# Kernel optimization log

Hardware: AMD Instinct MI355X
Metric: run time of the kernel (lower is better)

The kernel has to match this reference:

```python
import jax, jax.numpy as jnp
import numpy as np

N = 50000
E = 800000
IN_DIM = 128
HIDDEN = 128
OUT_DIM = 64
NUM_GRAPHS = 64


def setup_inputs() -> dict:
    key = jax.random.key(0)
    ks = jax.random.split(key, 16)
    x = jax.random.normal(ks[0], (N, IN_DIM), dtype=jnp.float32)
    edge_index = jax.random.randint(ks[1], (2, E), 0, N, dtype=jnp.int32)
    batch = jnp.sort(jax.random.randint(ks[2], (N,), 0, NUM_GRAPHS, dtype=jnp.int32))

    def glorot(k, shape):
        fan_in = shape[1]
        return jax.random.normal(k, shape, dtype=jnp.float32) / jnp.sqrt(jnp.float32(fan_in))

    # SAGEConv params: lin_l (on aggregated neighbors, with bias), lin_r (on self, no bias)
    return {
        "x": x,
        "edge_index": edge_index,
        "batch": batch,
        "W1l": glorot(ks[3], (HIDDEN, IN_DIM)), "b1l": jnp.zeros((HIDDEN,), jnp.float32),
        "W1r": glorot(ks[4], (HIDDEN, IN_DIM)),
        "W2l": glorot(ks[5], (HIDDEN, HIDDEN)), "b2l": jnp.zeros((HIDDEN,), jnp.float32),
        "W2r": glorot(ks[6], (HIDDEN, HIDDEN)),
        "W3l": glorot(ks[7], (HIDDEN, HIDDEN)), "b3l": jnp.zeros((HIDDEN,), jnp.float32),
        "W3r": glorot(ks[8], (HIDDEN, HIDDEN)),
        "Wlin": glorot(ks[9], (OUT_DIM, HIDDEN)), "blin": jnp.zeros((OUT_DIM,), jnp.float32),
    }


def sage_conv(x, src, dst, Wl, bl, Wr):
    # aggr='add': scatter-add source features onto target nodes, then two linears.
    agg = jax.ops.segment_sum(x[src], dst, num_segments=N)  # [N, d_in]
    return agg @ Wl.T + bl + x @ Wr.T


def reference(x, edge_index, batch, W1l, b1l, W1r, W2l, b2l, W2r, W3l, b3l, W3r, Wlin, blin):
    src, dst = edge_index[0], edge_index[1]
    h = jax.nn.relu(sage_conv(x, src, dst, W1l, b1l, W1r))
    # dropout p=0.3 is identity at inference
    h = jax.nn.relu(sage_conv(h, src, dst, W2l, b2l, W2r))
    h = sage_conv(h, src, dst, W3l, b3l, W3r)
    # global mean pool over graphs
    sums = jax.ops.segment_sum(h, batch, num_segments=NUM_GRAPHS)  # [G, hidden]
    counts = jax.ops.segment_sum(jnp.ones((N,), h.dtype), batch, num_segments=NUM_GRAPHS)
    pooled = sums / jnp.maximum(counts, 1.0)[:, None]
    return pooled @ Wlin.T + blin  # [G, out_dim]
```

## Files before the change

kernel.cpp:

```cpp
#include <hip/hip_runtime.h>


typedef __bf16 bf16x8 __attribute__((ext_vector_type(8)));
typedef float f32x4 __attribute__((ext_vector_type(4)));
typedef float f32x2 __attribute__((ext_vector_type(2)));

#define BINB 160
#define NBMAX 512
#define CH 8192

static __device__ __forceinline__ unsigned short f2bf(float f) {
    unsigned u = __builtin_bit_cast(unsigned, f);
    return (unsigned short)((u + 0x7fffu + ((u >> 16) & 1u)) >> 16);
}
static __device__ __forceinline__ uint2 pk8_fp8(const float* f) {
    int lo = 0, hi = 0;
    lo = __builtin_amdgcn_cvt_pk_fp8_f32(f[0], f[1], lo, false);
    lo = __builtin_amdgcn_cvt_pk_fp8_f32(f[2], f[3], lo, true);
    hi = __builtin_amdgcn_cvt_pk_fp8_f32(f[4], f[5], hi, false);
    hi = __builtin_amdgcn_cvt_pk_fp8_f32(f[6], f[7], hi, true);
    return make_uint2((unsigned)lo, (unsigned)hi);
}
static __device__ __forceinline__ unsigned char f2fp8(float v) {
    return (unsigned char)(__builtin_amdgcn_cvt_pk_fp8_f32(v, v, 0, false) & 0xff);
}

__global__ __launch_bounds__(256) void k_bincast(
    const int* __restrict__ ei, int* __restrict__ cnt_mat, int E, int nb, int epb,
    const float* __restrict__ x, unsigned short* __restrict__ xb,
    unsigned char* __restrict__ x8, int n8, int nxblk,
    const float* __restrict__ W1l, const float* __restrict__ W1r,
    const float* __restrict__ W2l, const float* __restrict__ W2r,
    unsigned short* __restrict__ Whi)
{
    __shared__ int lc[NBMAX];
    int bid = blockIdx.x;
    if (bid < BINB) {
        for (int i = threadIdx.x; i < nb; i += 256) lc[i] = 0;
        __syncthreads();
        int b0 = bid * epb;
        int b1 = min(b0 + epb, E);
        for (int i = b0 + threadIdx.x; i < b1; i += 256)
            atomicAdd(&lc[ei[E + i] >> 7], 1);
        __syncthreads();
        for (int i = threadIdx.x; i < nb; i += 256)
            cnt_mat[i * BINB + bid] = lc[i];
    } else if (bid < BINB + nxblk) {
        int i = (bid - BINB) * 256 + threadIdx.x;
        if (i >= n8) return;
        float f[8];
        *(float4*)(f + 0) = *(const float4*)(x + (size_t)i * 8);
        *(float4*)(f + 4) = *(const float4*)(x + (size_t)i * 8 + 4);
        ushort4 oa, ob;
        oa.x = f2bf(f[0]); oa.y = f2bf(f[1]); oa.z = f2bf(f[2]); oa.w = f2bf(f[3]);
        ob.x = f2bf(f[4]); ob.y = f2bf(f[5]); ob.z = f2bf(f[6]); ob.w = f2bf(f[7]);
        int node = i >> 4, c = i & 15;
        size_t dstb = (size_t)(node >> 4) * 2048 + (size_t)(c >> 2) * 512
                    + (size_t)((c & 3) * 16 + (node & 15)) * 8;
        *(ushort4*)(xb + dstb) = oa;
        *(ushort4*)(xb + dstb + 4) = ob;
        *(uint2*)(x8 + (size_t)i * 8) = pk8_fp8(f);
    } else {
        int wb = bid - BINB - nxblk;
        int layer = wb >> 7;
        int j = wb & 127;
        int k = threadIdx.x;
        const float* Wl = (layer == 0) ? W1l : W2l;
        const float* Wr = (layer == 0) ? W1r : W2r;
        float w = (k < 128) ? Wl[j * 128 + k] : Wr[j * 128 + k - 128];
        int js = j >> 4, mr = j & 15;
        int s = k >> 5, quad = (k >> 3) & 3, e = k & 7;
        size_t o = (size_t)layer * 32768
                 + ((size_t)(js * 8 + s) * 64 + quad * 16 + mr) * 8 + e;
        Whi[o] = f2bf(w);
    }
}

__global__ __launch_bounds__(256) void k_mrowscan(
    const int* __restrict__ cnt_mat, int* __restrict__ rowloc, int* __restrict__ btot)
{
    __shared__ int s[256];
    int b = blockIdx.x;
    int t = threadIdx.x;
    int v = (t < BINB) ? cnt_mat[b * BINB + t] : 0;
    s[t] = v;
    __syncthreads();
#pragma unroll
    for (int off = 1; off < 256; off <<= 1) {
        int u = (t >= off) ? s[t - off] : 0;
        __syncthreads();
        s[t] += u;
        __syncthreads();
    }
    if (t < BINB) rowloc[b * BINB + t] = s[t] - v;
    if (t == 255) btot[b] = s[255];
}

__global__ __launch_bounds__(256) void k_scan2b(
    const int* __restrict__ btot, int* __restrict__ bbase, int nb, int* __restrict__ total_out)
{
    __shared__ int s[256];
    int t = threadIdx.x;
    int per = (nb + 255) / 256;
    int s0 = t * per, e0 = min(s0 + per, nb);
    int sum = 0;
    for (int i = s0; i < e0; ++i) sum += btot[i];
    s[t] = sum;
    __syncthreads();
#pragma unroll
    for (int off = 1; off < 256; off <<= 1) {
        int u = (t >= off) ? s[t - off] : 0;
        __syncthreads();
        s[t] += u;
        __syncthreads();
    }
    int run = s[t] - sum;
    for (int i = s0; i < e0; ++i) { bbase[i] = run; run += btot[i]; }
    if (t == 255) *total_out = s[255];
}

__global__ __launch_bounds__(256) void k_binscatter(
    const int* __restrict__ ei, const int* __restrict__ rowloc, const int* __restrict__ bbase,
    unsigned* __restrict__ binned, int E, int nb, int epb)
{
    __shared__ int lofs[NBMAX];
    __shared__ int lcnt[NBMAX];
    for (int i = threadIdx.x; i < nb; i += 256) {
        lofs[i] = rowloc[i * BINB + blockIdx.x] + bbase[i];
        lcnt[i] = 0;
    }
    __syncthreads();
    int b0 = blockIdx.x * epb;
    int b1 = min(b0 + epb, E);
    for (int i = b0 + threadIdx.x; i < b1; i += 256) {
        int s = ei[i];
        int d = ei[E + i];
        int b = d >> 7;
        int r = atomicAdd(&lcnt[b], 1);
        binned[lofs[b] + r] = (unsigned)s | ((unsigned)(d & 127) << 16);
    }
}

__global__ __launch_bounds__(256) void k_fillfine2(
    const unsigned* __restrict__ binned, const int* __restrict__ bbase,
    const int* __restrict__ batch, int* __restrict__ starts,
    unsigned short* __restrict__ csr_src, int* __restrict__ gestart,
    int E, int nb, int n)
{
    __shared__ int lc[128];
    __shared__ int lpos[128];
    int b = blockIdx.x;
    int t = threadIdx.x;
    int node0 = b << 7;
    int bs = bbase[b];
    int be = (b == nb - 1) ? E : bbase[b + 1];
    if (t < 128) lc[t] = 0;
    __syncthreads();
    for (int i = bs + t; i < be; i += 256)
        atomicAdd(&lc[(binned[i] >> 16) & 127], 1);
    __syncthreads();
    int v = (t < 128) ? lc[t] : 0;
    if (t < 128) lpos[t] = v;
    __syncthreads();
#pragma unroll
    for (int off = 1; off < 128; off <<= 1) {
        int u = (t >= off && t < 128) ? lpos[t - off] : 0;
        __syncthreads();
        if (t < 128) lpos[t] += u;
        __syncthreads();
    }
    int excl = (t < 128) ? (lpos[t] - v) : 0;
    __syncthreads();
    if (t < 128) {
        int node = node0 + t;
        if (node < n) {
            int st = bs + excl;
            starts[node] = st;
            int bc = batch[node];
            int bp = (node == 0) ? -1 : batch[node - 1];
            for (int g = bp + 1; g <= bc; ++g) gestart[g] = st;
            if (node == n - 1)
                for (int g = bc + 1; g <= 64; ++g) gestart[g] = E;
        }
        lpos[t] = bs + excl;
    }
    if (b == nb - 1 && t == 0) starts[n] = E;
    __syncthreads();
    for (int i = bs + t; i < be; i += 256) {
        unsigned e = binned[i];
        int slot = atomicAdd(&lpos[(e >> 16) & 127], 1);
        csr_src[slot] = (unsigned short)(e & 0xffffu);
    }
}

__global__ __launch_bounds__(256) void k_hist(
    const unsigned short* __restrict__ csr, const int* __restrict__ gestart,
    const int* __restrict__ batch, unsigned short* __restrict__ cntb,
    int n, int nsp, int nch)
{
    __shared__ unsigned lc[CH];
    int bid = blockIdx.x;
    int c = bid % nch;
    int gr = bid / nch;
    int s0 = c * CH;
    int t = threadIdx.x;
    if (gr < 64) {
        for (int i = t; i < CH; i += 256) lc[i] = 0;
        __syncthreads();
        int e0 = gestart[gr], e1 = gestart[gr + 1];
        for (int i = e0 + t; i < e1; i += 256) {
            unsigned d = (unsigned)((int)csr[i] - s0);
            if (d < (unsigned)CH) atomicAdd(&lc[d], 1u);
        }
        __syncthreads();
        for (int i = t; i < CH; i += 256) {
            int s = s0 + i;
            if (s < nsp)
                cntb[(size_t)gr * nsp + s] = f2bf((float)lc[i]);
        }
    } else {
        int g2 = gr - 64;
        for (int i = t; i < CH; i += 256) {
            int s = s0 + i;
            if (s < nsp)
                cntb[(size_t)gr * nsp + s] =
                    (s < n && batch[s] == g2) ? (unsigned short)0x3f80 : (unsigned short)0;
        }
    }
}

#define ACC8P(v)                                                        \
    do {                                                                \
        f32x2 p0 = __builtin_amdgcn_cvt_pk_f32_fp8((v).x, false);       \
        f32x2 p1 = __builtin_amdgcn_cvt_pk_f32_fp8((v).x, true);        \
        f32x2 p2 = __builtin_amdgcn_cvt_pk_f32_fp8((v).y, false);       \
        f32x2 p3 = __builtin_amdgcn_cvt_pk_f32_fp8((v).y, true);        \
        A01 += p0; A23 += p1; A45 += p2; A67 += p3;                     \
    } while (0)

#define PROC_CHUNK(idxv, cntv)                                          \
    {                                                                   \
        int j = 0;                                                      \
        for (; j + 16 <= (cntv); j += 16) {                             \
            int s0 = __shfl((int)(idxv), j + eg);                       \
            int s1 = __shfl((int)(idxv), j + 4 + eg);                   \
            int s2 = __shfl((int)(idxv), j + 8 + eg);                   \
            int s3 = __shfl((int)(idxv), j + 12 + eg);                  \
            uint2 v0 = *(const uint2*)(hrow + (size_t)s0 * 128);        \
            uint2 v1 = *(const uint2*)(hrow + (size_t)s1 * 128);        \
            uint2 v2 = *(const uint2*)(hrow + (size_t)s2 * 128);        \
            uint2 v3 = *(const uint2*)(hrow + (size_t)s3 * 128);        \
            ACC8P(v0);                                                  \
            ACC8P(v1);                                                  \
            ACC8P(v2);                                                  \
            ACC8P(v3);                                                  \
        }                                                               \
        for (; j + 4 <= (cntv); j += 4) {                               \
            int s0 = __shfl((int)(idxv), j + eg);                       \
            uint2 v0 = *(const uint2*)(hrow + (size_t)s0 * 128);        \
            ACC8P(v0);                                                  \
        }                                                               \
        if (j < (cntv)) {                                               \
            int k = j + eg;                                             \
            int sm = __shfl((int)(idxv), (k < (cntv)) ? k : ((cntv) - 1)); \
            uint2 v = *(const uint2*)(hrow + (size_t)sm * 128);         \
            if (k >= (cntv)) v = make_uint2(0u, 0u);                    \
            ACC8P(v);                                                   \
        }                                                               \
    }

#define REDUCE8()                                                       \
    a0 += __shfl_xor(a0, 16); a0 += __shfl_xor(a0, 32);                 \
    a1 += __shfl_xor(a1, 16); a1 += __shfl_xor(a1, 32);                 \
    a2 += __shfl_xor(a2, 16); a2 += __shfl_xor(a2, 32);                 \
    a3 += __shfl_xor(a3, 16); a3 += __shfl_xor(a3, 32);                 \
    a4 += __shfl_xor(a4, 16); a4 += __shfl_xor(a4, 32);                 \
    a5 += __shfl_xor(a5, 16); a5 += __shfl_xor(a5, 32);                 \
    a6 += __shfl_xor(a6, 16); a6 += __shfl_xor(a6, 32);                 \
    a7 += __shfl_xor(a7, 16); a7 += __shfl_xor(a7, 32);

__global__ __launch_bounds__(256) void k_layer(
    const unsigned char* __restrict__ h8_in, const int* __restrict__ starts,
    const unsigned short* __restrict__ csr, const unsigned short* __restrict__ hf,
    const unsigned short* __restrict__ Whi, const float* __restrict__ bl,
    unsigned short* __restrict__ outf, unsigned char* __restrict__ out8,
    unsigned short* __restrict__ h2tb,
    int n, int nsp, int mode)
{
    __shared__ unsigned short sagg[2048];
    __shared__ unsigned char s8[2048];
    int t = threadIdx.x;
    int wv = t >> 6;
    int lane = t & 63;
    int node0 = blockIdx.x * 16;

    {
        int eg = lane >> 4;
        int fb = lane & 15;
        const unsigned char* hrow = h8_in + fb * 8;
        int nodeA = node0 + wv * 4;
        int st[5];
#pragma unroll
        for (int r = 0; r < 5; ++r) {
            int nn = nodeA + r;
            st[r] = starts[nn > n ? n : nn];
        }
        unsigned idx4[4];
#pragma unroll
        for (int r = 0; r < 4; ++r)
            idx4[r] = (st[r] + lane < st[r + 1]) ? (unsigned)csr[st[r] + lane] : 0u;

#pragma unroll
        for (int r = 0; r < 4; ++r) {
            f32x2 A01 = (f32x2){0.f, 0.f}, A23 = (f32x2){0.f, 0.f},
                  A45 = (f32x2){0.f, 0.f}, A67 = (f32x2){0.f, 0.f};
            int deg = st[r + 1] - st[r];
            int c0 = min(64, deg);
            PROC_CHUNK(idx4[r], c0)
            for (int base = st[r] + 64; base < st[r + 1]; base += 64) {
                int cnt2 = min(64, st[r + 1] - base);
                unsigned idx = (base + lane < st[r + 1]) ? (unsigned)csr[base + lane] : 0u;
                PROC_CHUNK(idx, cnt2)
            }
            float a0 = A01.x, a1 = A01.y, a2 = A23.x, a3 = A23.y,
                  a4 = A45.x, a5 = A45.y, a6 = A67.x, a7 = A67.y;
            REDUCE8()
            if (eg == 0) {
                int ln = wv * 4 + r;
                unsigned u0 = (unsigned)f2bf(a0) | ((unsigned)f2bf(a1) << 16);
                unsigned u1 = (unsigned)f2bf(a2) | ((unsigned)f2bf(a3) << 16);
                unsigned u2 = (unsigned)f2bf(a4) | ((unsigned)f2bf(a5) << 16);
                unsigned u3 = (unsigned)f2bf(a6) | ((unsigned)f2bf(a7) << 16);
                size_t dst = (size_t)(fb >> 2) * 512 + (size_t)((fb & 3) * 16 + ln) * 8;
                *(uint4*)(sagg + dst) = make_uint4(u0, u1, u2, u3);
            }
        }
    }
    __syncthreads();

    int quad = lane >> 4;
    int mr = lane & 15;
    int js0 = wv * 2;

    f32x4 acc0 = (f32x4){0.f, 0.f, 0.f, 0.f};
    f32x4 acc1 = (f32x4){0.f, 0.f, 0.f, 0.f};

    const unsigned short* wp = Whi + (size_t)js0 * 4096 + (size_t)lane * 8;
    const unsigned short* sa = sagg + (size_t)lane * 8;
    const unsigned short* ha = hf + (size_t)blockIdx.x * 2048 + (size_t)lane * 8;

    uint4 pb[2][3];
#define LAYER_LOAD(s, b)                                                  \
    do {                                                                  \
        pb[b][0] = *(const uint4*)(wp + (size_t)(s) * 512);               \
        pb[b][1] = *(const uint4*)(wp + 4096 + (size_t)(s) * 512);        \
        pb[b][2] = ((s) < 4)                                              \
            ? *(const uint4*)(sa + (size_t)(s) * 512)                     \
            : *(const uint4*)(ha + (size_t)((s) - 4) * 512);              \
    } while (0)

    LAYER_LOAD(0, 0);
    LAYER_LOAD(1, 1);
#pragma unroll
    for (int s = 0; s < 8; ++s) {
        int b = s & 1;
        bf16x8 bh0 = __builtin_bit_cast(bf16x8, pb[b][0]);
        bf16x8 bh1 = __builtin_bit_cast(bf16x8, pb[b][1]);
        bf16x8 A0 = __builtin_bit_cast(bf16x8, pb[b][2]);
        acc0 = __builtin_amdgcn_mfma_f32_16x16x32_bf16(A0, bh0, acc0, 0, 0, 0);
        acc1 = __builtin_amdgcn_mfma_f32_16x16x32_bf16(A0, bh1, acc1, 0, 0, 0);
        if (s + 2 < 8) LAYER_LOAD(s + 2, b);
    }
#undef LAYER_LOAD

    float vv[2][4];
#pragma unroll
    for (int mi = 0; mi < 2; ++mi) {
        f32x4 a = mi ? acc1 : acc0;
        int col = (js0 + mi) * 16 + mr;
        float bias = bl[col];
#pragma unroll
        for (int r = 0; r < 4; ++r) {
            int node = node0 + quad * 4 + r;
            float v = fmaxf(a[r] + bias, 0.f);
            vv[mi][r] = (node < n) ? v : 0.f;
        }
    }
    __syncthreads();
    if (mode == 0) {
#pragma unroll
        for (int mi = 0; mi < 2; ++mi) {
            int col = (js0 + mi) * 16 + mr;
            int so = col >> 5, q2 = (col >> 3) & 3, e2 = col & 7;
#pragma unroll
            for (int r = 0; r < 4; ++r) {
                int nl = quad * 4 + r;
                sagg[so * 512 + (q2 * 16 + nl) * 8 + e2] = f2bf(vv[mi][r]);
                s8[nl * 128 + col] = f2fp8(vv[mi][r]);
            }
        }
        __syncthreads();
        *(uint4*)(outf + (size_t)blockIdx.x * 2048 + (size_t)t * 8) =
            *(const uint4*)(sagg + (size_t)t * 8);
        int nl = t >> 4;
        if (node0 + nl < n)
            *(uint2*)(out8 + (size_t)(node0 + nl) * 128 + (t & 15) * 8) =
                *(const uint2*)(s8 + nl * 128 + (t & 15) * 8);
    } else {
#pragma unroll
        for (int mi = 0; mi < 2; ++mi) {
            int col = (js0 + mi) * 16 + mr;
#pragma unroll
            for (int r = 0; r < 4; ++r)
                sagg[col * 16 + quad * 4 + r] = f2bf(vv[mi][r]);
        }
        __syncthreads();
        int col = t >> 1;
        *(uint4*)(h2tb + (size_t)col * nsp + node0 + (t & 1) * 8) =
            *(const uint4*)(sagg + col * 16 + (t & 1) * 8);
    }
}

__global__ __launch_bounds__(256) void k_gsum(
    const unsigned short* __restrict__ cntb, const unsigned short* __restrict__ h2tb,
    float* __restrict__ part, int nsp, int ksteps, int gb)
{
    int t = threadIdx.x;
    int wv = t >> 6, lane = t & 63;
    int fast = lane & 15;
    int kc = (lane >> 4) * 8;
    int kpb = (ksteps + gb - 1) / gb;
    int k0 = blockIdx.x * kpb, k1 = min(k0 + kpb, ksteps);

    f32x4 accE[8], accP[8];
#pragma unroll
    for (int i = 0; i < 8; ++i) {
        accE[i] = (f32x4){0.f, 0.f, 0.f, 0.f};
        accP[i] = (f32x4){0.f, 0.f, 0.f, 0.f};
    }

    const unsigned short* apE = cntb + (size_t)(wv * 16 + fast) * nsp + kc;
    const unsigned short* apP = apE + (size_t)64 * nsp;
    const unsigned short* bp  = h2tb + (size_t)fast * nsp + kc;

    if (k0 < k1) {
        int kb = k0 * 32;
        uint4 ca0 = *(const uint4*)(apE + kb);
        uint4 ca1 = *(const uint4*)(apP + kb);
        uint4 cb[8];
#pragma unroll
        for (int ft = 0; ft < 8; ++ft)
            cb[ft] = *(const uint4*)(bp + (size_t)ft * 16 * nsp + kb);
        for (int ks = k0; ks < k1; ++ks) {
            int kn = min(ks + 1, k1 - 1) * 32;
            uint4 na0 = *(const uint4*)(apE + kn);
            uint4 na1 = *(const uint4*)(apP + kn);
            uint4 nb[8];
#pragma unroll
            for (int ft = 0; ft < 8; ++ft)
                nb[ft] = *(const uint4*)(bp + (size_t)ft * 16 * nsp + kn);
            bf16x8 aE = __builtin_bit_cast(bf16x8, ca0);
            bf16x8 aP = __builtin_bit_cast(bf16x8, ca1);
#pragma unroll
            for (int ft = 0; ft < 8; ++ft) {
                bf16x8 bf = __builtin_bit_cast(bf16x8, cb[ft]);
                accE[ft] = __builtin_amdgcn_mfma_f32_16x16x32_bf16(aE, bf, accE[ft], 0, 0, 0);
                accP[ft] = __builtin_amdgcn_mfma_f32_16x16x32_bf16(aP, bf, accP[ft], 0, 0, 0);
            }
            ca0 = na0; ca1 = na1;
#pragma unroll
            for (int ft = 0; ft < 8; ++ft) cb[ft] = nb[ft];
        }
    }
    float* po = part + (size_t)blockIdx.x * 16384;
    int quad = lane >> 4, mr = lane & 15;
#pragma unroll
    for (int ft = 0; ft < 8; ++ft) {
        int col = ft * 16 + mr;
#pragma unroll
        for (int r = 0; r < 4; ++r) {
            po[(size_t)(wv * 16 + quad * 4 + r) * 128 + col] = accE[ft][r];
            po[(size_t)(64 + wv * 16 + quad * 4 + r) * 128 + col] = accP[ft][r];
        }
    }
}

__global__ __launch_bounds__(256) void k_reduce(
    const float* __restrict__ part, float* __restrict__ red, int gb)
{
    int i = blockIdx.x * 256 + threadIdx.x;
    float s0 = 0.f, s1 = 0.f, s2 = 0.f, s3 = 0.f;
    int p = 0;
    for (; p + 4 <= gb; p += 4) {
        s0 += part[(size_t)p * 16384 + i];
        s1 += part[(size_t)(p + 1) * 16384 + i];
        s2 += part[(size_t)(p + 2) * 16384 + i];
        s3 += part[(size_t)(p + 3) * 16384 + i];
    }
    for (; p < gb; ++p) s0 += part[(size_t)p * 16384 + i];
    red[i] = (s0 + s1) + (s2 + s3);
}

__global__ __launch_bounds__(128) void k_final(
    const float* __restrict__ red, const int* __restrict__ batch,
    const float* __restrict__ W3l, const float* __restrict__ b3,
    const float* __restrict__ W3r,
    const float* __restrict__ Wlin, const float* __restrict__ blin,
    float* __restrict__ out, int n)
{
    __shared__ float sE[128], sP[128], tmp[128];
    int g = blockIdx.x;
    int t = threadIdx.x;
    sE[t] = red[g * 128 + t];
    sP[t] = red[(64 + g) * 128 + t];

    int lo = 0, hi = n;
    while (lo < hi) { int m = (lo + hi) >> 1; if (batch[m] < g) lo = m + 1; else hi = m; }
    int lb = lo;
    hi = n;
    while (lo < hi) { int m = (lo + hi) >> 1; if (batch[m] < g + 1) lo = m + 1; else hi = m; }
    int cnt = lo - lb;
    float inv = (cnt > 0) ? 1.f / (float)cnt : 0.f;
    __syncthreads();

    float acc = 0.f;
    for (int k = 0; k < 128; ++k)
        acc += sE[k] * W3l[t * 128 + k] + sP[k] * W3r[t * 128 + k];
    tmp[t] = acc * inv + ((cnt > 0) ? b3[t] : 0.f);
    __syncthreads();

    if (t < 64) {
        float o = 0.f;
        for (int k = 0; k < 128; ++k)
            o += tmp[k] * Wlin[t * 128 + k];
        out[g * 64 + t] = o + blin[t];
    }
}

extern "C" void kernel_launch(void* const* d_in, const int* in_sizes, int n_in,
                              void* d_out, int out_size, void* d_ws, size_t ws_size,
                              hipStream_t stream) {
    const float* x     = (const float*)d_in[0];
    const int*   ei    = (const int*)d_in[1];
    const int*   batch = (const int*)d_in[2];
    const float* W1l = (const float*)d_in[3];
    const float* b1l = (const float*)d_in[4];
    const float* W1r = (const float*)d_in[5];
    const float* W2l = (const float*)d_in[6];
    const float* b2l = (const float*)d_in[7];
    const float* W2r = (const float*)d_in[8];
    const float* W3l = (const float*)d_in[9];
    const float* b3l = (const float*)d_in[10];
    const float* W3r = (const float*)d_in[11];
    const float* Wlin = (const float*)d_in[12];
    const float* blin = (const float*)d_in[13];

    const int N = in_sizes[2];
    const int E = in_sizes[1] / 2;
    const int nb = (N + 127) >> 7;
    const int epb = (E + BINB - 1) / BINB;
    const int NSP = ((N + 31) / 32) * 32;
    const int KSTEPS = NSP / 32;
    const int NCH = (NSP + CH - 1) / CH;
    const int GB = 128;

    size_t off = 0;
    auto alloc = [&](size_t bytes) {
        void* p = (char*)d_ws + off;
        off += (bytes + 255) & ~(size_t)255;
        return p;
    };
    int* csr_start = (int*)alloc((size_t)(N + 1) * 4);
    int* cnt_mat   = (int*)alloc((size_t)nb * BINB * 4);
    int* rowloc    = (int*)alloc((size_t)nb * BINB * 4);
    int* btot      = (int*)alloc((size_t)NBMAX * 4);
    int* bbase     = (int*)alloc((size_t)NBMAX * 4);
    int* gestart   = (int*)alloc(256 + 64);
    unsigned short* csr_src = (unsigned short*)alloc((size_t)E * 2);
    unsigned*       binned  = (unsigned*)alloc((size_t)E * 4);
    unsigned short* x_bf = (unsigned short*)alloc((size_t)N * 128 * 2 + 65536);
    unsigned short* hA   = (unsigned short*)alloc((size_t)N * 128 * 2 + 65536);
    unsigned char*  x8   = (unsigned char*)alloc((size_t)N * 128);
    unsigned char*  h1_8 = (unsigned char*)alloc((size_t)N * 128);
    unsigned short* h2Tb = (unsigned short*)alloc((size_t)128 * NSP * 2);
    unsigned short* cntb = (unsigned short*)alloc((size_t)128 * NSP * 2);
    unsigned short* Whi  = (unsigned short*)alloc(2 * 128 * 256 * 2);
    float*          part = (float*)alloc((size_t)GB * 16384 * 4);
    float*          red  = (float*)alloc((size_t)16384 * 4);
    (void)ws_size;

    int n8 = N * 128 / 8;
    int nxblk = (n8 + 255) / 256;
    k_bincast<<<BINB + nxblk + 256, 256, 0, stream>>>(
        ei, cnt_mat, E, nb, epb,
        x, x_bf, x8, n8, nxblk, W1l, W1r, W2l, W2r, Whi);
    k_mrowscan<<<nb, 256, 0, stream>>>(cnt_mat, rowloc, btot);
    k_scan2b<<<1, 256, 0, stream>>>(btot, bbase, nb, csr_start + N);
    k_binscatter<<<BINB, 256, 0, stream>>>(ei, rowloc, bbase, binned, E, nb, epb);
    k_fillfine2<<<nb, 256, 0, stream>>>(binned, bbase, batch, csr_start, csr_src,
                                        gestart, E, nb, N);
    k_hist<<<128 * NCH, 256, 0, stream>>>(csr_src, gestart, batch, cntb, N, NSP, NCH);

    int lay_grid  = (N + 15) / 16;
    int lay2_grid = NSP / 16;

    k_layer<<<lay_grid, 256, 0, stream>>>(x8, csr_start, csr_src, x_bf,
                                          Whi, b1l, hA, h1_8, h2Tb, N, NSP, 0);
    k_layer<<<lay2_grid, 256, 0, stream>>>(h1_8, csr_start, csr_src, hA,
                                           Whi + 32768, b2l, hA, h1_8, h2Tb, N, NSP, 1);
    k_gsum<<<GB, 256, 0, stream>>>(cntb, h2Tb, part, NSP, KSTEPS, GB);
    k_reduce<<<64, 256, 0, stream>>>(part, red, GB);

    k_final<<<64, 128, 0, stream>>>(red, batch, W3l, b3l, W3r,
                                    Wlin, blin, (float*)d_out, N);
}
```

Baseline: 257.7 us.

## Fuse CSR binning into one pass with atomic bin offsets and merge histogram into layer

Result: slower. 578.8 us (+124.6%).

```diff
diff --git a/kernel.cpp b/kernel.cpp
--- a/kernel.cpp
+++ b/kernel.cpp
@@ -5,9 +5,10 @@
 typedef float f32x4 __attribute__((ext_vector_type(4)));
 typedef float f32x2 __attribute__((ext_vector_type(2)));
 
-#define BINB 160
 #define NBMAX 512
-#define CH 8192
+#define CH 4096
+#define NSB 160
+#define SSTRIDE 3072
 
 static __device__ __forceinline__ unsigned short f2bf(float f) {
     unsigned u = __builtin_bit_cast(unsigned, f);
@@ -25,46 +26,71 @@
     return (unsigned char)(__builtin_amdgcn_cvt_pk_fp8_f32(v, v, 0, false) & 0xff);
 }
 
-__global__ __launch_bounds__(256) void k_bincast(
-    const int* __restrict__ ei, int* __restrict__ cnt_mat, int E, int nb, int epb,
+__global__ __launch_bounds__(256) void k_scatcast(
+    const int* __restrict__ ei, unsigned* __restrict__ binned,
+    unsigned* __restrict__ gbcnt, int* __restrict__ bbase, unsigned* __restrict__ done,
+    int E, int nb, int epb,
     const float* __restrict__ x, unsigned short* __restrict__ xb,
     unsigned char* __restrict__ x8, int n8, int nxblk,
     const float* __restrict__ W1l, const float* __restrict__ W1r,
     const float* __restrict__ W2l, const float* __restrict__ W2r,
     unsigned short* __restrict__ Whi)
 {
-    __shared__ int lc[NBMAX];
+    __shared__ unsigned sedge[5120];
+    __shared__ int lcnt[NBMAX];
+    __shared__ int lofs[NBMAX];
+    __shared__ unsigned rank;
     int bid = blockIdx.x;
-    if (bid < BINB) {
-        for (int i = threadIdx.x; i < nb; i += 256) lc[i] = 0;
-        __syncthreads();
+    int t = threadIdx.x;
+
+    if (bid < NSB) {
         int b0 = bid * epb;
         int b1 = min(b0 + epb, E);
-        for (int i = b0 + threadIdx.x; i < b1; i += 256)
-            atomicAdd(&lc[ei[E + i] >> 7], 1);
-        __syncthreads();
-        for (int i = threadIdx.x; i < nb; i += 256)
-            cnt_mat[i * BINB + bid] = lc[i];
-    } else if (bid < BINB + nxblk) {
-        int i = (bid - BINB) * 256 + threadIdx.x;
-        if (i >= n8) return;
-        float f[8];
-        *(float4*)(f + 0) = *(const float4*)(x + (size_t)i * 8);
-        *(float4*)(f + 4) = *(const float4*)(x + (size_t)i * 8 + 4);
-        ushort4 oa, ob;
-        oa.x = f2bf(f[0]); oa.y = f2bf(f[1]); oa.z = f2bf(f[2]); oa.w = f2bf(f[3]);
-        ob.x = f2bf(f[4]); ob.y = f2bf(f[5]); ob.z = f2bf(f[6]); ob.w = f2bf(f[7]);
-        int node = i >> 4, c = i & 15;
-        size_t dstb = (size_t)(node >> 4) * 2048 + (size_t)(c >> 2) * 512
-                    + (size_t)((c & 3) * 16 + (node & 15)) * 8;
-        *(ushort4*)(xb + dstb) = oa;
-        *(ushort4*)(xb + dstb + 4) = ob;
-        *(uint2*)(x8 + (size_t)i * 8) = pk8_fp8(f);
+        int cnt = b1 - b0;
+        for (int i = t; i < nb; i += 256) lcnt[i] = 0;
+        __syncthreads();
+        for (int i = t; i < cnt; i += 256) {
+            int s = ei[b0 + i];
+            int d = ei[E + b0 + i];
+            sedge[i] = (unsigned)s | ((unsigned)(d & 127) << 16)
+                     | ((unsigned)(d >> 7) << 23);
+            atomicAdd(&lcnt[d >> 7], 1);
+        }
+        __syncthreads();
+        for (int i = t; i < nb; i += 256) {
+            int c = lcnt[i];
+            lofs[i] = (c > 0) ? (int)atomicAdd(&gbcnt[i], (unsigned)c) : 0;
+            lcnt[i] = 0;
+        }
+        __syncthreads();
+        for (int i = t; i < cnt; i += 256) {
+            unsigned e = sedge[i];
+            int b = e >> 23;
+            int r = lofs[b] + atomicAdd(&lcnt[b], 1);
+            if (r < SSTRIDE)
+                binned[(size_t)b * SSTRIDE + r] = e & 0x7fffffu;
+        }
+    } else if (bid < NSB + nxblk) {
+        int i = (bid - NSB) * 256 + t;
+        if (i < n8) {
+            float f[8];
+            *(float4*)(f + 0) = *(const float4*)(x + (size_t)i * 8);
+            *(float4*)(f + 4) = *(const float4*)(x + (size_t)i * 8 + 4);
+            ushort4 oa, ob;
+            oa.x = f2bf(f[0]); oa.y = f2bf(f[1]); oa.z = f2bf(f[2]); oa.w = f2bf(f[3]);
+            ob.x = f2bf(f[4]); ob.y = f2bf(f[5]); ob.z = f2bf(f[6]); ob.w = f2bf(f[7]);
+            int node = i >> 4, c = i & 15;
+            size_t dstb = (size_t)(node >> 4) * 2048 + (size_t)(c >> 2) * 512
+                        + (size_t)((c & 3) * 16 + (node & 15)) * 8;
+            *(ushort4*)(xb + dstb) = oa;
+            *(ushort4*)(xb + dstb + 4) = ob;
+            *(uint2*)(x8 + (size_t)i * 8) = pk8_fp8(f);
+        }
     } else {
-        int wb = bid - BINB - nxblk;
+        int wb = bid - NSB - nxblk;
         int layer = wb >> 7;
         int j = wb & 127;
-        int k = threadIdx.x;
+        int k = t;
         const float* Wl = (layer == 0) ? W1l : W2l;
         const float* Wr = (layer == 0) ? W1r : W2r;
         float w = (k < 128) ? Wl[j * 128 + k] : Wr[j * 128 + k - 128];
@@ -74,75 +100,34 @@
                  + ((size_t)(js * 8 + s) * 64 + quad * 16 + mr) * 8 + e;
         Whi[o] = f2bf(w);
     }
-}
-
-__global__ __launch_bounds__(256) void k_mrowscan(
-    const int* __restrict__ cnt_mat, int* __restrict__ rowloc, int* __restrict__ btot)
-{
-    __shared__ int s[256];
-    int b = blockIdx.x;
-    int t = threadIdx.x;
-    int v = (t < BINB) ? cnt_mat[b * BINB + t] : 0;
-    s[t] = v;
-    __syncthreads();
-#pragma unroll
-    for (int off = 1; off < 256; off <<= 1) {
-        int u = (t >= off) ? s[t - off] : 0;
-        __syncthreads();
-        s[t] += u;
-        __syncthreads();
-    }
-    if (t < BINB) rowloc[b * BINB + t] = s[t] - v;
-    if (t == 255) btot[b] = s[255];
-}
-
-__global__ __launch_bounds__(256) void k_scan2b(
-    const int* __restrict__ btot, int* __restrict__ bbase, int nb, int* __restrict__ total_out)
-{
-    __shared__ int s[256];
-    int t = threadIdx.x;
-    int per = (nb + 255) / 256;
-    int s0 = t * per, e0 = min(s0 + per, nb);
-    int sum = 0;
-    for (int i = s0; i < e0; ++i) sum += btot[i];
-    s[t] = sum;
-    __syncthreads();
-#pragma unroll
-    for (int off = 1; off < 256; off <<= 1) {
-        int u = (t >= off) ? s[t - off] : 0;
-        __syncthreads();
-        s[t] += u;
-        __syncthreads();
-    }
-    int run = s[t] - sum;
-    for (int i = s0; i < e0; ++i) { bbase[i] = run; run += btot[i]; }
-    if (t == 255) *total_out = s[255];
-}
-
-__global__ __launch_bounds__(256) void k_binscatter(
-    const int* __restrict__ ei, const int* __restrict__ rowloc, const int* __restrict__ bbase,
-    unsigned* __restrict__ binned, int E, int nb, int epb)
-{
-    __shared__ int lofs[NBMAX];
-    __shared__ int lcnt[NBMAX];
-    for (int i = threadIdx.x; i < nb; i += 256) {
-        lofs[i] = rowloc[i * BINB + blockIdx.x] + bbase[i];
-        lcnt[i] = 0;
-    }
-    __syncthreads();
-    int b0 = blockIdx.x * epb;
-    int b1 = min(b0 + epb, E);
-    for (int i = b0 + threadIdx.x; i < b1; i += 256) {
-        int s = ei[i];
-        int d = ei[E + i];
-        int b = d >> 7;
-        int r = atomicAdd(&lcnt[b], 1);
-        binned[lofs[b] + r] = (unsigned)s | ((unsigned)(d & 127) << 16);
+
+    __syncthreads();
+    __threadfence();
+    if (t == 0) rank = atomicAdd(done, 1u);
+    __syncthreads();
+    if (rank == gridDim.x - 1) {
+        __shared__ int ss[512];
+        int c0 = (t < nb) ? (int)gbcnt[t] : 0;
+        int c1 = (256 + t < nb) ? (int)gbcnt[256 + t] : 0;
+        ss[t] = c0;
+        ss[256 + t] = c1;
+        __syncthreads();
+        for (int off2 = 1; off2 < 512; off2 <<= 1) {
+            int a0 = (t >= off2) ? ss[t - off2] : 0;
+            int a1 = (t + 256 >= off2) ? ss[t + 256 - off2] : 0;
+            __syncthreads();
+            ss[t] += a0;
+            ss[t + 256] += a1;
+            __syncthreads();
+        }
+        if (t < nb) bbase[t] = ss[t] - c0;
+        if (256 + t < nb) bbase[256 + t] = ss[256 + t] - c1;
     }
 }
 
 __global__ __launch_bounds__(256) void k_fillfine2(
-    const unsigned* __restrict__ binned, const int* __restrict__ bbase,
+    const unsigned* __restrict__ binned, const unsigned* __restrict__ gbcnt,
+    const int* __restrict__ bbase,
     const int* __restrict__ batch, int* __restrict__ starts,
     unsigned short* __restrict__ csr_src, int* __restrict__ gestart,
     int E, int nb, int n)
@@ -152,8 +137,9 @@
     int b = blockIdx.x;
     int t = threadIdx.x;
     int node0 = b << 7;
-    int bs = bbase[b];
-    int be = (b == nb - 1) ? E : bbase[b + 1];
+    int bs = b * SSTRIDE;
+    int be = bs + (int)gbcnt[b];
+    int wb = bbase[b];
     if (t < 128) lc[t] = 0;
     __syncthreads();
     for (int i = bs + t; i < be; i += 256)
@@ -174,7 +160,7 @@
     if (t < 128) {
         int node = node0 + t;
         if (node < n) {
-            int st = bs + excl;
+            int st = wb + excl;
             starts[node] = st;
             int bc = batch[node];
             int bp = (node == 0) ? -1 : batch[node - 1];
@@ -182,7 +168,7 @@
             if (node == n - 1)
                 for (int g = bc + 1; g <= 64; ++g) gestart[g] = E;
         }
-        lpos[t] = bs + excl;
+        lpos[t] = wb + excl;
     }
     if (b == nb - 1 && t == 0) starts[n] = E;
     __syncthreads();
@@ -190,42 +176,6 @@
         unsigned e = binned[i];
         int slot = atomicAdd(&lpos[(e >> 16) & 127], 1);
         csr_src[slot] = (unsigned short)(e & 0xffffu);
-    }
-}
-
-__global__ __launch_bounds__(256) void k_hist(
-    const unsigned short* __restrict__ csr, const int* __restrict__ gestart,
-    const int* __restrict__ batch, unsigned short* __restrict__ cntb,
-    int n, int nsp, int nch)
-{
-    __shared__ unsigned lc[CH];
-    int bid = blockIdx.x;
-    int c = bid % nch;
-    int gr = bid / nch;
-    int s0 = c * CH;
-    int t = threadIdx.x;
-    if (gr < 64) {
-        for (int i = t; i < CH; i += 256) lc[i] = 0;
-        __syncthreads();
-        int e0 = gestart[gr], e1 = gestart[gr + 1];
-        for (int i = e0 + t; i < e1; i += 256) {
-            unsigned d = (unsigned)((int)csr[i] - s0);
-            if (d < (unsigned)CH) atomicAdd(&lc[d], 1u);
-        }
-        __syncthreads();
-        for (int i = t; i < CH; i += 256) {
-            int s = s0 + i;
-            if (s < nsp)
-                cntb[(size_t)gr * nsp + s] = f2bf((float)lc[i]);
-        }
-    } else {
-        int g2 = gr - 64;
-        for (int i = t; i < CH; i += 256) {
-            int s = s0 + i;
-            if (s < nsp)
-                cntb[(size_t)gr * nsp + s] =
-                    (s < n && batch[s] == g2) ? (unsigned short)0x3f80 : (unsigned short)0;
-        }
     }
 }
 
@@ -285,11 +235,48 @@
     const unsigned short* __restrict__ Whi, const float* __restrict__ bl,
     unsigned short* __restrict__ outf, unsigned char* __restrict__ out8,
     unsigned short* __restrict__ h2tb,
-    int n, int nsp, int mode)
+    const int* __restrict__ gestart, const int* __restrict__ batch,
+    unsigned short* __restrict__ cntb,
+    int n, int nsp, int mode, int laygrid, int nch)
 {
-    __shared__ unsigned short sagg[2048];
-    __shared__ unsigned char s8[2048];
+    __shared__ unsigned smem[CH];
+    unsigned short* sagg = (unsigned short*)smem;
+    unsigned char*  s8   = (unsigned char*)(smem + 1024);
     int t = threadIdx.x;
+
+    if ((int)blockIdx.x >= laygrid) {
+        unsigned* lc = smem;
+        int hb = blockIdx.x - laygrid;
+        int c = hb % nch;
+        int gr = hb / nch;
+        int s0 = c * CH;
+        if (gr < 64) {
+            for (int i = t; i < CH; i += 256) lc[i] = 0;
+            __syncthreads();
+            int e0 = gestart[gr], e1 = gestart[gr + 1];
+            for (int i = e0 + t; i < e1; i += 256) {
+                unsigned d = (unsigned)((int)csr[i] - s0);
+                if (d < (unsigned)CH) atomicAdd(&lc[d], 1u);
+            }
+            __syncthreads();
+            for (int i = t; i < CH; i += 256) {
+                int s = s0 + i;
+                if (s < nsp)
+                    cntb[(size_t)gr * nsp + s] = f2bf((float)lc[i]);
+            }
+        } else {
+            int g2 = gr - 64;
+            for (int i = t; i < CH; i += 256) {
+                int s = s0 + i;
+                if (s < nsp)
+                    cntb[(size_t)gr * nsp + s] =
+                        (s < n && batch[s] == g2) ? (unsigned short)0x3f80
+                                                  : (unsigned short)0;
+            }
+        }
+        return;
+    }
+
     int wv = t >> 6;
     int lane = t & 63;
     int node0 = blockIdx.x * 16;
@@ -558,7 +545,7 @@
     const int N = in_sizes[2];
     const int E = in_sizes[1] / 2;
     const int nb = (N + 127) >> 7;
-    const int epb = (E + BINB - 1) / BINB;
+    const int epb = (E + NSB - 1) / NSB;
     const int NSP = ((N + 31) / 32) * 32;
     const int KSTEPS = NSP / 32;
     const int NCH = (NSP + CH - 1) / CH;
@@ -571,13 +558,12 @@
         return p;
     };
     int* csr_start = (int*)alloc((size_t)(N + 1) * 4);
-    int* cnt_mat   = (int*)alloc((size_t)nb * BINB * 4);
-    int* rowloc    = (int*)alloc((size_t)nb * BINB * 4);
-    int* btot      = (int*)alloc((size_t)NBMAX * 4);
-    int* bbase     = (int*)alloc((size_t)NBMAX * 4);
-    int* gestart   = (int*)alloc(256 + 64);
+    unsigned* gbcnt = (unsigned*)alloc((size_t)NBMAX * 4);
+    unsigned* done  = (unsigned*)alloc(256);
+    int* bbase      = (int*)alloc((size_t)NBMAX * 4);
+    int* gestart    = (int*)alloc(256 + 64);
     unsigned short* csr_src = (unsigned short*)alloc((size_t)E * 2);
-    unsigned*       binned  = (unsigned*)alloc((size_t)E * 4);
+    unsigned*       binned  = (unsigned*)alloc((size_t)nb * SSTRIDE * 4);
     unsigned short* x_bf = (unsigned short*)alloc((size_t)N * 128 * 2 + 65536);
     unsigned short* hA   = (unsigned short*)alloc((size_t)N * 128 * 2 + 65536);
     unsigned char*  x8   = (unsigned char*)alloc((size_t)N * 128);
@@ -589,28 +575,29 @@
     float*          red  = (float*)alloc((size_t)16384 * 4);
     (void)ws_size;
 
+    hipMemsetAsync(gbcnt, 0, (size_t)NBMAX * 4 + 256, stream);
+
     int n8 = N * 128 / 8;
     int nxblk = (n8 + 255) / 256;
-    k_bincast<<<BINB + nxblk + 256, 256, 0, stream>>>(
-        ei, cnt_mat, E, nb, epb,
+
+    k_scatcast<<<NSB + nxblk + 256, 256, 0, stream>>>(
+        ei, binned, gbcnt, bbase, done, E, nb, epb,
         x, x_bf, x8, n8, nxblk, W1l, W1r, W2l, W2r, Whi);
-    k_mrowscan<<<nb, 256, 0, stream>>>(cnt_mat, rowloc, btot);
-    k_scan2b<<<1, 256, 0, stream>>>(btot, bbase, nb, csr_start + N);
-    k_binscatter<<<BINB, 256, 0, stream>>>(ei, rowloc, bbase, binned, E, nb, epb);
-    k_fillfine2<<<nb, 256, 0, stream>>>(binned, bbase, batch, csr_start, csr_src,
-                                        gestart, E, nb, N);
-    k_hist<<<128 * NCH, 256, 0, stream>>>(csr_src, gestart, batch, cntb, N, NSP, NCH);
+    k_fillfine2<<<nb, 256, 0, stream>>>(binned, gbcnt, bbase, batch,
+                                        csr_start, csr_src, gestart, E, nb, N);
 
     int lay_grid  = (N + 15) / 16;
     int lay2_grid = NSP / 16;
-
-    k_layer<<<lay_grid, 256, 0, stream>>>(x8, csr_start, csr_src, x_bf,
-                                          Whi, b1l, hA, h1_8, h2Tb, N, NSP, 0);
-    k_layer<<<lay2_grid, 256, 0, stream>>>(h1_8, csr_start, csr_src, hA,
-                                           Whi + 32768, b2l, hA, h1_8, h2Tb, N, NSP, 1);
+    int hist_grid = 128 * NCH;
+
+    k_layer<<<lay_grid + hist_grid, 256, 0, stream>>>(
+        x8, csr_start, csr_src, x_bf, Whi, b1l, hA, h1_8, h2Tb,
+        gestart, batch, cntb, N, NSP, 0, lay_grid, NCH);
+    k_layer<<<lay2_grid, 256, 0, stream>>>(
+        h1_8, csr_start, csr_src, hA, Whi + 32768, b2l, hA, h1_8, h2Tb,
+        gestart, batch, cntb, N, NSP, 1, lay2_grid, 1);
     k_gsum<<<GB, 256, 0, stream>>>(cntb, h2Tb, part, NSP, KSTEPS, GB);
     k_reduce<<<64, 256, 0, stream>>>(part, red, GB);
-
     k_final<<<64, 128, 0, stream>>>(red, batch, W3l, b3l, W3r,
                                     Wlin, blin, (float*)d_out, N);
 }
```

## Fuse histogram into layer kernel, widen blocks to 512, tile h2 layout

Applied to the files above, without the earlier changes.

Measured after the change: 234.8 us. 1.1x faster.

```diff
diff --git a/kernel.cpp b/kernel.cpp
--- a/kernel.cpp
+++ b/kernel.cpp
@@ -7,7 +7,7 @@
 
 #define BINB 160
 #define NBMAX 512
-#define CH 8192
+#define CH 4096
 
 static __device__ __forceinline__ unsigned short f2bf(float f) {
     unsigned u = __builtin_bit_cast(unsigned, f);
@@ -193,42 +193,6 @@
     }
 }
 
-__global__ __launch_bounds__(256) void k_hist(
-    const unsigned short* __restrict__ csr, const int* __restrict__ gestart,
-    const int* __restrict__ batch, unsigned short* __restrict__ cntb,
-    int n, int nsp, int nch)
-{
-    __shared__ unsigned lc[CH];
-    int bid = blockIdx.x;
-    int c = bid % nch;
-    int gr = bid / nch;
-    int s0 = c * CH;
-    int t = threadIdx.x;
-    if (gr < 64) {
-        for (int i = t; i < CH; i += 256) lc[i] = 0;
-        __syncthreads();
-        int e0 = gestart[gr], e1 = gestart[gr + 1];
-        for (int i = e0 + t; i < e1; i += 256) {
-            unsigned d = (unsigned)((int)csr[i] - s0);
-            if (d < (unsigned)CH) atomicAdd(&lc[d], 1u);
-        }
-        __syncthreads();
-        for (int i = t; i < CH; i += 256) {
-            int s = s0 + i;
-            if (s < nsp)
-                cntb[(size_t)gr * nsp + s] = f2bf((float)lc[i]);
-        }
-    } else {
-        int g2 = gr - 64;
-        for (int i = t; i < CH; i += 256) {
-            int s = s0 + i;
-            if (s < nsp)
-                cntb[(size_t)gr * nsp + s] =
-                    (s < n && batch[s] == g2) ? (unsigned short)0x3f80 : (unsigned short)0;
-        }
-    }
-}
-
 #define ACC8P(v)                                                        \
     do {                                                                \
         f32x2 p0 = __builtin_amdgcn_cvt_pk_f32_fp8((v).x, false);       \
@@ -279,17 +243,54 @@
     a6 += __shfl_xor(a6, 16); a6 += __shfl_xor(a6, 32);                 \
     a7 += __shfl_xor(a7, 16); a7 += __shfl_xor(a7, 32);
 
-__global__ __launch_bounds__(256) void k_layer(
+__global__ __launch_bounds__(512) void k_layer(
     const unsigned char* __restrict__ h8_in, const int* __restrict__ starts,
     const unsigned short* __restrict__ csr, const unsigned short* __restrict__ hf,
     const unsigned short* __restrict__ Whi, const float* __restrict__ bl,
     unsigned short* __restrict__ outf, unsigned char* __restrict__ out8,
     unsigned short* __restrict__ h2tb,
-    int n, int nsp, int mode)
-{
-    __shared__ unsigned short sagg[2048];
-    __shared__ unsigned char s8[2048];
+    const int* __restrict__ gestart, const int* __restrict__ batch,
+    unsigned short* __restrict__ cntb,
+    int n, int nsp, int mode, int laygrid, int nch)
+{
+    __shared__ unsigned smem[CH];
+    unsigned short* sagg = (unsigned short*)smem;
+    unsigned char*  s8   = (unsigned char*)(smem + 1024);
     int t = threadIdx.x;
+
+    if ((int)blockIdx.x >= laygrid) {
+        unsigned* lc = smem;
+        int hb = blockIdx.x - laygrid;
+        int c = hb % nch;
+        int gr = hb / nch;
+        int s0 = c * CH;
+        if (gr < 64) {
+            for (int i = t; i < CH; i += 512) lc[i] = 0;
+            __syncthreads();
+            int e0 = gestart[gr], e1 = gestart[gr + 1];
+            for (int i = e0 + t; i < e1; i += 512) {
+                unsigned d = (unsigned)((int)csr[i] - s0);
+                if (d < (unsigned)CH) atomicAdd(&lc[d], 1u);
+            }
+            __syncthreads();
+            for (int i = t; i < CH; i += 512) {
+                int s = s0 + i;
+                if (s < nsp)
+                    cntb[(size_t)gr * nsp + s] = f2bf((float)lc[i]);
+            }
+        } else {
+            int g2 = gr - 64;
+            for (int i = t; i < CH; i += 512) {
+                int s = s0 + i;
+                if (s < nsp)
+                    cntb[(size_t)gr * nsp + s] =
+                        (s < n && batch[s] == g2) ? (unsigned short)0x3f80
+                                                  : (unsigned short)0;
+            }
+        }
+        return;
+    }
+
     int wv = t >> 6;
     int lane = t & 63;
     int node0 = blockIdx.x * 16;
@@ -298,25 +299,25 @@
         int eg = lane >> 4;
         int fb = lane & 15;
         const unsigned char* hrow = h8_in + fb * 8;
-        int nodeA = node0 + wv * 4;
-        int st[5];
-#pragma unroll
-        for (int r = 0; r < 5; ++r) {
+        int nodeA = node0 + wv * 2;
+        int st[3];
+#pragma unroll
+        for (int r = 0; r < 3; ++r) {
             int nn = nodeA + r;
             st[r] = starts[nn > n ? n : nn];
         }
-        unsigned idx4[4];
-#pragma unroll
-        for (int r = 0; r < 4; ++r)
-            idx4[r] = (st[r] + lane < st[r + 1]) ? (unsigned)csr[st[r] + lane] : 0u;
-
-#pragma unroll
-        for (int r = 0; r < 4; ++r) {
+        unsigned idx2[2];
+#pragma unroll
+        for (int r = 0; r < 2; ++r)
+            idx2[r] = (st[r] + lane < st[r + 1]) ? (unsigned)csr[st[r] + lane] : 0u;
+
+#pragma unroll
+        for (int r = 0; r < 2; ++r) {
             f32x2 A01 = (f32x2){0.f, 0.f}, A23 = (f32x2){0.f, 0.f},
                   A45 = (f32x2){0.f, 0.f}, A67 = (f32x2){0.f, 0.f};
             int deg = st[r + 1] - st[r];
             int c0 = min(64, deg);
-            PROC_CHUNK(idx4[r], c0)
+            PROC_CHUNK(idx2[r], c0)
             for (int base = st[r] + 64; base < st[r + 1]; base += 64) {
                 int cnt2 = min(64, st[r + 1] - base);
                 unsigned idx = (base + lane < st[r + 1]) ? (unsigned)csr[base + lane] : 0u;
@@ -326,7 +327,7 @@
                   a4 = A45.x, a5 = A45.y, a6 = A67.x, a7 = A67.y;
             REDUCE8()
             if (eg == 0) {
-                int ln = wv * 4 + r;
+                int ln = wv * 2 + r;
                 unsigned u0 = (unsigned)f2bf(a0) | ((unsigned)f2bf(a1) << 16);
                 unsigned u1 = (unsigned)f2bf(a2) | ((unsigned)f2bf(a3) << 16);
                 unsigned u2 = (unsigned)f2bf(a4) | ((unsigned)f2bf(a5) << 16);
@@ -340,21 +341,19 @@
 
     int quad = lane >> 4;
     int mr = lane & 15;
-    int js0 = wv * 2;
-
-    f32x4 acc0 = (f32x4){0.f, 0.f, 0.f, 0.f};
-    f32x4 acc1 = (f32x4){0.f, 0.f, 0.f, 0.f};
-
-    const unsigned short* wp = Whi + (size_t)js0 * 4096 + (size_t)lane * 8;
+    int js = wv;
+
+    f32x4 acc = (f32x4){0.f, 0.f, 0.f, 0.f};
+
+    const unsigned short* wp = Whi + (size_t)js * 4096 + (size_t)lane * 8;
     const unsigned short* sa = sagg + (size_t)lane * 8;
     const unsigned short* ha = hf + (size_t)blockIdx.x * 2048 + (size_t)lane * 8;
 
-    uint4 pb[2][3];
+    uint4 pb[2][2];
 #define LAYER_LOAD(s, b)                                                  \
     do {                                                                  \
         pb[b][0] = *(const uint4*)(wp + (size_t)(s) * 512);               \
-        pb[b][1] = *(const uint4*)(wp + 4096 + (size_t)(s) * 512);        \
-        pb[b][2] = ((s) < 4)                                              \
+        pb[b][1] = ((s) < 4)                                              \
             ? *(const uint4*)(sa + (size_t)(s) * 512)                     \
             : *(const uint4*)(ha + (size_t)((s) - 4) * 512);              \
     } while (0)
@@ -364,60 +363,45 @@
 #pragma unroll
     for (int s = 0; s < 8; ++s) {
         int b = s & 1;
-        bf16x8 bh0 = __builtin_bit_cast(bf16x8, pb[b][0]);
-        bf16x8 bh1 = __builtin_bit_cast(bf16x8, pb[b][1]);
-        bf16x8 A0 = __builtin_bit_cast(bf16x8, pb[b][2]);
-        acc0 = __builtin_amdgcn_mfma_f32_16x16x32_bf16(A0, bh0, acc0, 0, 0, 0);
-        acc1 = __builtin_amdgcn_mfma_f32_16x16x32_bf16(A0, bh1, acc1, 0, 0, 0);
+        bf16x8 bh = __builtin_bit_cast(bf16x8, pb[b][0]);
+        bf16x8 A0 = __builtin_bit_cast(bf16x8, pb[b][1]);
+        acc = __builtin_amdgcn_mfma_f32_16x16x32_bf16(A0, bh, acc, 0, 0, 0);
         if (s + 2 < 8) LAYER_LOAD(s + 2, b);
     }
 #undef LAYER_LOAD
 
-    float vv[2][4];
-#pragma unroll
-    for (int mi = 0; mi < 2; ++mi) {
-        f32x4 a = mi ? acc1 : acc0;
-        int col = (js0 + mi) * 16 + mr;
-        float bias = bl[col];
+    int col = js * 16 + mr;
+    float bias = bl[col];
+    float vv[4];
+#pragma unroll
+    for (int r = 0; r < 4; ++r) {
+        int node = node0 + quad * 4 + r;
+        float v = fmaxf(acc[r] + bias, 0.f);
+        vv[r] = (node < n) ? v : 0.f;
+    }
+    __syncthreads();
+    if (mode == 0) {
+        int so = col >> 5, q2 = (col >> 3) & 3, e2 = col & 7;
 #pragma unroll
         for (int r = 0; r < 4; ++r) {
-            int node = node0 + quad * 4 + r;
-            float v = fmaxf(a[r] + bias, 0.f);
-            vv[mi][r] = (node < n) ? v : 0.f;
+            int nl = quad * 4 + r;
+            sagg[so * 512 + (q2 * 16 + nl) * 8 + e2] = f2bf(vv[r]);
+            s8[nl * 128 + col] = f2fp8(vv[r]);
         }
-    }
-    __syncthreads();
-    if (mode == 0) {
-#pragma unroll
-        for (int mi = 0; mi < 2; ++mi) {
-            int col = (js0 + mi) * 16 + mr;
-            int so = col >> 5, q2 = (col >> 3) & 3, e2 = col & 7;
-#pragma unroll
-            for (int r = 0; r < 4; ++r) {
-                int nl = quad * 4 + r;
-                sagg[so * 512 + (q2 * 16 + nl) * 8 + e2] = f2bf(vv[mi][r]);
-                s8[nl * 128 + col] = f2fp8(vv[mi][r]);
-            }
-        }
-        __syncthreads();
-        *(uint4*)(outf + (size_t)blockIdx.x * 2048 + (size_t)t * 8) =
-            *(const uint4*)(sagg + (size_t)t * 8);
-        int nl = t >> 4;
+        __syncthreads();
+        *(uint2*)(outf + (size_t)blockIdx.x * 2048 + (size_t)t * 4) =
+            *(const uint2*)(sagg + (size_t)t * 4);
+        int nl = t >> 5;
         if (node0 + nl < n)
-            *(uint2*)(out8 + (size_t)(node0 + nl) * 128 + (t & 15) * 8) =
-                *(const uint2*)(s8 + nl * 128 + (t & 15) * 8);
+            *(unsigned*)(out8 + (size_t)(node0 + nl) * 128 + (t & 31) * 4) =
+                *(const unsigned*)(s8 + nl * 128 + (t & 31) * 4);
     } else {
 #pragma unroll
-        for (int mi = 0; mi < 2; ++mi) {
-            int col = (js0 + mi) * 16 + mr;
-#pragma unroll
-            for (int r = 0; r < 4; ++r)
-                sagg[col * 16 + quad * 4 + r] = f2bf(vv[mi][r]);
-        }
-        __syncthreads();
-        int col = t >> 1;
-        *(uint4*)(h2tb + (size_t)col * nsp + node0 + (t & 1) * 8) =
-            *(const uint4*)(sagg + col * 16 + (t & 1) * 8);
+        for (int r = 0; r < 4; ++r)
+            sagg[col * 16 + quad * 4 + r] = f2bf(vv[r]);
+        __syncthreads();
+        *(uint2*)(h2tb + (size_t)blockIdx.x * 2048 + (size_t)t * 4) =
+            *(const uint2*)(sagg + (size_t)t * 4);
     }
 }
 
@@ -441,24 +425,26 @@
 
     const unsigned short* apE = cntb + (size_t)(wv * 16 + fast) * nsp + kc;
     const unsigned short* apP = apE + (size_t)64 * nsp;
-    const unsigned short* bp  = h2tb + (size_t)fast * nsp + kc;
 
     if (k0 < k1) {
-        int kb = k0 * 32;
-        uint4 ca0 = *(const uint4*)(apE + kb);
-        uint4 ca1 = *(const uint4*)(apP + kb);
+        int kk = k0 * 32 + kc;
+        const unsigned short* bt = h2tb + ((size_t)(kk >> 4)) * 2048 + (kk & 15);
+        uint4 ca0 = *(const uint4*)(apE + k0 * 32);
+        uint4 ca1 = *(const uint4*)(apP + k0 * 32);
         uint4 cb[8];
 #pragma unroll
         for (int ft = 0; ft < 8; ++ft)
-            cb[ft] = *(const uint4*)(bp + (size_t)ft * 16 * nsp + kb);
+            cb[ft] = *(const uint4*)(bt + (size_t)(fast + ft * 16) * 16);
         for (int ks = k0; ks < k1; ++ks) {
-            int kn = min(ks + 1, k1 - 1) * 32;
-            uint4 na0 = *(const uint4*)(apE + kn);
-            uint4 na1 = *(const uint4*)(apP + kn);
+            int ksn = min(ks + 1, k1 - 1);
+            int kkn = ksn * 32 + kc;
+            const unsigned short* btn = h2tb + ((size_t)(kkn >> 4)) * 2048 + (kkn & 15);
+            uint4 na0 = *(const uint4*)(apE + ksn * 32);
+            uint4 na1 = *(const uint4*)(apP + ksn * 32);
             uint4 nb[8];
 #pragma unroll
             for (int ft = 0; ft < 8; ++ft)
-                nb[ft] = *(const uint4*)(bp + (size_t)ft * 16 * nsp + kn);
+                nb[ft] = *(const uint4*)(btn + (size_t)(fast + ft * 16) * 16);
             bf16x8 aE = __builtin_bit_cast(bf16x8, ca0);
             bf16x8 aP = __builtin_bit_cast(bf16x8, ca1);
 #pragma unroll
@@ -599,18 +585,19 @@
     k_binscatter<<<BINB, 256, 0, stream>>>(ei, rowloc, bbase, binned, E, nb, epb);
     k_fillfine2<<<nb, 256, 0, stream>>>(binned, bbase, batch, csr_start, csr_src,
                                         gestart, E, nb, N);
-    k_hist<<<128 * NCH, 256, 0, stream>>>(csr_src, gestart, batch, cntb, N, NSP, NCH);
 
     int lay_grid  = (N + 15) / 16;
     int lay2_grid = NSP / 16;
-
-    k_layer<<<lay_grid, 256, 0, stream>>>(x8, csr_start, csr_src, x_bf,
-                                          Whi, b1l, hA, h1_8, h2Tb, N, NSP, 0);
-    k_layer<<<lay2_grid, 256, 0, stream>>>(h1_8, csr_start, csr_src, hA,
-                                           Whi + 32768, b2l, hA, h1_8, h2Tb, N, NSP, 1);
+    int hist_grid = 128 * NCH;
+
+    k_layer<<<lay_grid + hist_grid, 512, 0, stream>>>(
+        x8, csr_start, csr_src, x_bf, Whi, b1l, hA, h1_8, h2Tb,
+        gestart, batch, cntb, N, NSP, 0, lay_grid, NCH);
+    k_layer<<<lay2_grid, 512, 0, stream>>>(
+        h1_8, csr_start, csr_src, hA, Whi + 32768, b2l, hA, h1_8, h2Tb,
+        gestart, batch, cntb, N, NSP, 1, lay2_grid, 1);
     k_gsum<<<GB, 256, 0, stream>>>(cntb, h2Tb, part, NSP, KSTEPS, GB);
     k_reduce<<<64, 256, 0, stream>>>(part, red, GB);
-
     k_final<<<64, 128, 0, stream>>>(red, batch, W3l, b3l, W3r,
                                     Wlin, blin, (float*)d_out, N);
 }
```
